# Kernel tuning notes

Hardware: AMD Instinct MI355X
Metric: run time of the kernel (lower is better)

Reference implementation:

```python
import jax, jax.numpy as jnp
import numpy as np

EMBED_DIM = 1024
N_HEADS = 16
HEAD_DIM = EMBED_DIM // N_HEADS
N_CATS = 5
SCALE = float(np.sqrt(HEAD_DIM))


def setup_inputs() -> dict:
    key = jax.random.key(0)
    ks = jax.random.split(key, 16)
    B, S = 2, 2048
    inp = {
        "query": jax.random.normal(ks[0], (B, S, EMBED_DIM), jnp.float32),
        "key_": jax.random.normal(ks[1], (B, S, EMBED_DIM), jnp.float32),
        "value": jax.random.normal(ks[2], (B, S, EMBED_DIM), jnp.float32),
        "responses": jax.random.randint(ks[3], (B, S), 0, N_CATS),
        "mask": jnp.ones((B, S, S), jnp.int32),
        # Linear params (torch convention: y = x @ W.T + b)
        "Wq": jax.random.normal(ks[4], (EMBED_DIM, EMBED_DIM), jnp.float32) * 0.02,
        "bq": jnp.zeros((EMBED_DIM,), jnp.float32),
        "Wk": jax.random.normal(ks[5], (EMBED_DIM, EMBED_DIM), jnp.float32) * 0.02,
        "bk": jnp.zeros((EMBED_DIM,), jnp.float32),
        "Wv": jax.random.normal(ks[6], (EMBED_DIM, EMBED_DIM), jnp.float32) * 0.02,
        "bv": jnp.zeros((EMBED_DIM,), jnp.float32),
        "Wo": jax.random.normal(ks[7], (EMBED_DIM, EMBED_DIM), jnp.float32) * 0.02,
        "bo": jnp.zeros((EMBED_DIM,), jnp.float32),
        # qwk_modulation: Linear(1, n_heads)
        "Wm": jax.random.normal(ks[8], (N_HEADS, 1), jnp.float32) * 0.5,
        "bm": jnp.zeros((N_HEADS,), jnp.float32),
    }
    return inp


def _qwk_matrix():
    i = jnp.arange(N_CATS, dtype=jnp.float32)
    return 1.0 - (i[:, None] - i[None, :]) ** 2 / (N_CATS - 1) ** 2  # [C, C]


def reference(query, key_, value, responses, mask,
              Wq, bq, Wk, bk, Wv, bv, Wo, bo, Wm, bm):
    B, S, E = query.shape
    # projections
    Q = (query @ Wq.T + bq).reshape(B, S, N_HEADS, HEAD_DIM).transpose(0, 2, 1, 3)
    K = (key_ @ Wk.T + bk).reshape(B, S, N_HEADS, HEAD_DIM).transpose(0, 2, 1, 3)
    V = (value @ Wv.T + bv).reshape(B, S, N_HEADS, HEAD_DIM).transpose(0, 2, 1, 3)
    scores = jnp.einsum("bhqd,bhkd->bhqk", Q, K) / SCALE  # [B,H,S,S]
    # QWK ordinal bias: gather pairwise weight, tiny linear 1->H, broadcast-add
    qwk = _qwk_matrix()
    pair = qwk[responses[:, :, None], responses[:, None, :]]  # [B,S,S]
    # Linear(1, n_heads): bias[...,None] @ Wm.T + bm -> [B,S,S,H] -> [B,H,S,S]
    head_bias = pair[:, None, :, :] * Wm[:, 0][None, :, None, None] + bm[None, :, None, None]
    scores = scores + head_bias
    scores = jnp.where(mask[:, None, :, :] == 0, -1e9, scores)
    attn = jax.nn.softmax(scores, axis=-1)
    attended = jnp.einsum("bhqk,bhkd->bhqd", attn, V)
    attended = attended.transpose(0, 2, 1, 3).reshape(B, S, E)
    return attended @ Wo.T + bo
```

## Files before the change

### kernel.cpp

```cpp
#include <hip/hip_runtime.h>
#include <hip/hip_bf16.h>
#include <stdint.h>

#define S_LEN 2048
#define EMB   1024
#define NHEAD 16
#define HDIM  64
#define BATCH 2

typedef __bf16 bf16x8 __attribute__((ext_vector_type(8)));
typedef float  f32x4  __attribute__((ext_vector_type(4)));

__device__ __forceinline__ void gll16(const void* g, void* l) {
  __builtin_amdgcn_global_load_lds(
      (const __attribute__((address_space(1))) void*)g,
      (__attribute__((address_space(3))) void*)l,
      16, 0, 0);
}

__global__ void __launch_bounds__(256) cast_mask_kernel(
    const float* __restrict__ s0, const float* __restrict__ s1, const float* __restrict__ s2,
    const float* __restrict__ s3, const float* __restrict__ s4, const float* __restrict__ s5,
    const float* __restrict__ s6,
    __hip_bfloat16* __restrict__ d0, __hip_bfloat16* __restrict__ d1,
    __hip_bfloat16* __restrict__ d2, __hip_bfloat16* __restrict__ d3,
    __hip_bfloat16* __restrict__ d4, __hip_bfloat16* __restrict__ d5,
    __hip_bfloat16* __restrict__ d6,
    const int* __restrict__ mask, unsigned* __restrict__ flags) {
  const int z = blockIdx.y;
  const int t = threadIdx.x;
  if (z == 7) {
    const int kt = blockIdx.x & 15, qt = (blockIdx.x >> 4) & 31, b = (int)blockIdx.x >> 9;
    const int* base = mask + ((size_t)b * S_LEN + (size_t)qt * 64) * S_LEN + (size_t)kt * 128;
    int ok = 1;
#pragma unroll
    for (int p = 0; p < 8; ++p) {
      int idx = p * 256 + t;
      int row = idx >> 5, c4 = idx & 31;
      const int4 v = *(const int4*)(base + (size_t)row * S_LEN + c4 * 4);
      ok &= (v.x != 0) & (v.y != 0) & (v.z != 0) & (v.w != 0);
    }
    unsigned long long bl = __ballot(ok);
    __shared__ unsigned long long bw[4];
    bw[t >> 6] = bl;
    __syncthreads();
    if (t == 0) {
      unsigned all = ((bw[0] & bw[1] & bw[2] & bw[3]) == ~0ull) ? 1u : 0u;
      flags[((size_t)b * 32 + qt) * 16 + kt] = all;
    }
    return;
  }
  const float* s = (z == 0) ? s0 : (z == 1) ? s1 : (z == 2) ? s2 : (z == 3) ? s3
                 : (z == 4) ? s4 : (z == 5) ? s5 : s6;
  __hip_bfloat16* d = (z == 0) ? d0 : (z == 1) ? d1 : (z == 2) ? d2 : (z == 3) ? d3
                    : (z == 4) ? d4 : (z == 5) ? d5 : d6;
  const int n = (z < 3) ? (BATCH * S_LEN * EMB) : (EMB * EMB);
  const size_t i = ((size_t)blockIdx.x * 256 + t) * 16;
  if (i >= (size_t)n) return;
  __hip_bfloat16 tmp[16];
#pragma unroll
  for (int j = 0; j < 4; ++j) {
    const float4 v = *(const float4*)(s + i + j * 4);
    tmp[j * 4 + 0] = __float2bfloat16(v.x);
    tmp[j * 4 + 1] = __float2bfloat16(v.y);
    tmp[j * 4 + 2] = __float2bfloat16(v.z);
    tmp[j * 4 + 3] = __float2bfloat16(v.w);
  }
  *(bf16x8*)(d + i)     = *(bf16x8*)&tmp[0];
  *(bf16x8*)(d + i + 8) = *(bf16x8*)&tmp[8];
}

__global__ void __launch_bounds__(256, 2)
gemm_kernel(const __hip_bfloat16* __restrict__ A0, const __hip_bfloat16* __restrict__ A1,
            const __hip_bfloat16* __restrict__ A2,
            const __hip_bfloat16* __restrict__ W0, const __hip_bfloat16* __restrict__ W1,
            const __hip_bfloat16* __restrict__ W2,
            const float* __restrict__ b0, const float* __restrict__ b1,
            const float* __restrict__ b2,
            __hip_bfloat16* __restrict__ O0, __hip_bfloat16* __restrict__ O1,
            __hip_bfloat16* __restrict__ O2) {
  __shared__ __align__(16) __hip_bfloat16 As[128 * 32];
  __shared__ __align__(16) __hip_bfloat16 Bs[128 * 32];

  const int z = blockIdx.z;
  const __hip_bfloat16* A  = (z == 0) ? A0 : ((z == 1) ? A1 : A2);
  const __hip_bfloat16* W  = (z == 0) ? W0 : ((z == 1) ? W1 : W2);
  const float* bi          = (z == 0) ? b0 : ((z == 1) ? b1 : b2);
  __hip_bfloat16* O        = (z == 0) ? O0 : ((z == 1) ? O1 : O2);

  const int t = threadIdx.x;
  const int w = t >> 6, lane = t & 63, quad = lane >> 4, l15 = lane & 15;
  const int m0 = blockIdx.y * 128, n0 = blockIdx.x * 128;
  const int wr = w >> 1, wc = w & 1;

  f32x4 acc[4][4];
#pragma unroll
  for (int i = 0; i < 4; ++i)
#pragma unroll
    for (int j = 0; j < 4; ++j) acc[i][j] = (f32x4)0.0f;

  for (int k0 = 0; k0 < EMB; k0 += 32) {
    __syncthreads();
#pragma unroll
    for (int rnd = 0; rnd < 2; ++rnd) {
      int idx = rnd * 256 + t;
      gll16(A + (size_t)(m0 + (idx >> 2)) * EMB + k0 + ((idx & 3) << 3),
            &As[(rnd * 256 + (w << 6)) * 8]);
      gll16(W + (size_t)(n0 + (idx >> 2)) * EMB + k0 + ((idx & 3) << 3),
            &Bs[(rnd * 256 + (w << 6)) * 8]);
    }
    __syncthreads();

    bf16x8 af[4], bfr[4];
#pragma unroll
    for (int i = 0; i < 4; ++i)
      af[i] = *(const bf16x8*)&As[(wr * 64 + i * 16 + l15) * 32 + quad * 8];
#pragma unroll
    for (int j = 0; j < 4; ++j)
      bfr[j] = *(const bf16x8*)&Bs[(wc * 64 + j * 16 + l15) * 32 + quad * 8];
#pragma unroll
    for (int i = 0; i < 4; ++i)
#pragma unroll
      for (int j = 0; j < 4; ++j)
        acc[i][j] = __builtin_amdgcn_mfma_f32_16x16x32_bf16(af[i], bfr[j], acc[i][j], 0, 0, 0);
  }

#pragma unroll
  for (int j = 0; j < 4; ++j) {
    const int ng = n0 + wc * 64 + j * 16 + l15;
    const float bb = bi[ng];
    const int h = ng >> 6, d = ng & 63;
#pragma unroll
    for (int i = 0; i < 4; ++i) {
#pragma unroll
      for (int r = 0; r < 4; ++r) {
        const int mg = m0 + wr * 64 + i * 16 + quad * 4 + r;
        const int b = mg >> 11, s = mg & 2047;
        float v = acc[i][j][r] + bb;
        if (z == 0) {
          O[(((size_t)b * NHEAD + h) * S_LEN + s) * HDIM + d] =
              __float2bfloat16(v * (0.125f * 1.4426950408889634f));
        } else if (z == 1) {
          O[(((size_t)b * NHEAD + h) * S_LEN + s) * HDIM + d] = __float2bfloat16(v);
        } else {
          const size_t idx = (size_t)(b * NHEAD + h) * 131072 + (size_t)(s >> 7) * 8192 +
                             (size_t)((((s >> 5) & 3) * 4 + ((s >> 2) & 3)) * 64 + d) * 8 +
                             ((s >> 4) & 1) * 4 + (s & 3);
          O[idx] = __float2bfloat16(v);
        }
      }
    }
  }
}

__global__ void __launch_bounds__(256, 2)
gemm_o_kernel(const __hip_bfloat16* __restrict__ A, const __hip_bfloat16* __restrict__ W,
              const float* __restrict__ bi, float* __restrict__ O) {
  __shared__ __align__(16) __hip_bfloat16 As[64 * 32];
  __shared__ __align__(16) __hip_bfloat16 Bs[128 * 32];
  const int t = threadIdx.x;
  const int w = t >> 6, lane = t & 63, quad = lane >> 4, l15 = lane & 15;
  const int m0 = blockIdx.y * 64, n0 = blockIdx.x * 128;
  const int wr = w >> 1, wc = w & 1;

  f32x4 acc[2][4];
#pragma unroll
  for (int i = 0; i < 2; ++i)
#pragma unroll
    for (int j = 0; j < 4; ++j) acc[i][j] = (f32x4)0.0f;

  for (int k0 = 0; k0 < EMB; k0 += 32) {
    __syncthreads();
    gll16(A + (size_t)(m0 + (t >> 2)) * EMB + k0 + ((t & 3) << 3), &As[(w << 6) * 8]);
#pragma unroll
    for (int rnd = 0; rnd < 2; ++rnd) {
      int idx = rnd * 256 + t;
      gll16(W + (size_t)(n0 + (idx >> 2)) * EMB + k0 + ((idx & 3) << 3),
            &Bs[(rnd * 256 + (w << 6)) * 8]);
    }
    __syncthreads();

    bf16x8 af[2], bfr[4];
#pragma unroll
    for (int i = 0; i < 2; ++i)
      af[i] = *(const bf16x8*)&As[(wr * 32 + i * 16 + l15) * 32 + quad * 8];
#pragma unroll
    for (int j = 0; j < 4; ++j)
      bfr[j] = *(const bf16x8*)&Bs[(wc * 64 + j * 16 + l15) * 32 + quad * 8];
#pragma unroll
    for (int i = 0; i < 2; ++i)
#pragma unroll
      for (int j = 0; j < 4; ++j)
        acc[i][j] = __builtin_amdgcn_mfma_f32_16x16x32_bf16(af[i], bfr[j], acc[i][j], 0, 0, 0);
  }

#pragma unroll
  for (int j = 0; j < 4; ++j) {
    const int ng = n0 + wc * 64 + j * 16 + l15;
    const float bb = bi[ng];
#pragma unroll
    for (int i = 0; i < 2; ++i) {
#pragma unroll
      for (int r = 0; r < 4; ++r) {
        const int mg = m0 + wr * 32 + i * 16 + quad * 4 + r;
        O[(size_t)mg * EMB + ng] = acc[i][j][r] + bb;
      }
    }
  }
}

__global__ void __launch_bounds__(256, 4)
flash_kernel(const __hip_bfloat16* __restrict__ qws, const __hip_bfloat16* __restrict__ kws,
             const __hip_bfloat16* __restrict__ vpk, const int* __restrict__ responses,
             const int* __restrict__ mask, const float* __restrict__ Wm,
             const unsigned* __restrict__ flags, __hip_bfloat16* __restrict__ att) {
  __shared__ __align__(16) __hip_bfloat16 Ks[128 * 64];
  __shared__ __align__(16) __hip_bfloat16 Vs[8192];
  __shared__ unsigned char rb[S_LEN];

  const int t = threadIdx.x;
  const int w = t >> 6, lane = t & 63, quad = lane >> 4, l15 = lane & 15;
  const int qt = blockIdx.x, h = blockIdx.y, b = blockIdx.z;
  const int bh = b * NHEAD + h;
  const int q0 = qt * 64;

#pragma unroll
  for (int i = 0; i < 8; ++i)
    rb[i * 256 + t] = (unsigned char)responses[b * S_LEN + i * 256 + t];

  const __hip_bfloat16* qbase = qws + ((size_t)bh * S_LEN + q0) * HDIM;
  bf16x8 qf[2];
#pragma unroll
  for (int ks = 0; ks < 2; ++ks)
    qf[ks] = *(const bf16x8*)(qbase + (size_t)(w * 16 + l15) * HDIM + ks * 32 + quad * 8);

  const float c = Wm[h] * (0.0625f * 1.4426950408889634f);
  const float rqf = (float)responses[b * S_LEN + q0 + w * 16 + l15];
  const float A2 = 2.0f * c * rqf;

  const __hip_bfloat16* kptr = kws + ((size_t)bh * S_LEN + (t >> 3)) * HDIM +
                               (((t & 7) ^ ((t >> 3) & 7)) << 3);
  const __hip_bfloat16* vptr = vpk + (size_t)bh * 131072 + (size_t)t * 8;

  float lsum = 0.0f;
  f32x4 acc_o[4];
#pragma unroll
  for (int dt = 0; dt < 4; ++dt) acc_o[dt] = (f32x4)0.0f;

  for (int kt = 0; kt < S_LEN / 128; ++kt) {
    __syncthreads();
#pragma unroll
    for (int p = 0; p < 4; ++p) {
      gll16(kptr + p * 32 * HDIM, &Ks[(p * 256 + (w << 6)) * 8]);
      gll16(vptr + p * 2048,      &Vs[(p * 256 + (w << 6)) * 8]);
    }
    kptr += 128 * HDIM;
    vptr += 8192;
    __syncthreads();

    const unsigned fl = flags[((size_t)b * 32 + qt) * 16 + kt];

    bf16x8 pfr[4];
#pragma unroll
    for (int ct = 0; ct < 8; ++ct) {
      const int rowk = ct * 16 + l15;
      bf16x8 kf0 = *(const bf16x8*)&Ks[rowk * 64 + ((quad ^ (l15 & 7)) << 3)];
      bf16x8 kf1 = *(const bf16x8*)&Ks[rowk * 64 + (((4 + quad) ^ (l15 & 7)) << 3)];
      f32x4 sc = __builtin_amdgcn_mfma_f32_16x16x32_bf16(kf0, qf[0], (f32x4)0.0f, 0, 0, 0);
      sc = __builtin_amdgcn_mfma_f32_16x16x32_bf16(kf1, qf[1], sc, 0, 0, 0);

      const unsigned ru = *(const unsigned*)&rb[kt * 128 + ct * 16 + quad * 4];

      __hip_bfloat16 pb[4];
#pragma unroll
      for (int r = 0; r < 4; ++r) {
        const float rkf = (float)((ru >> (8 * r)) & 255u);
        const float tt = fmaf(-c, rkf, A2);
        const float sb = fmaf(rkf, tt, sc[r]);
        float p = __builtin_amdgcn_exp2f(sb);
        if (!fl) {
          int mq = mask[((size_t)b * S_LEN + q0 + w * 16 + l15) * S_LEN +
                        kt * 128 + ct * 16 + quad * 4 + r];
          p = mq ? p : 0.0f;
        }
        lsum += p;
        pb[r] = __float2bfloat16(p);
      }
      __hip_bfloat16* half = (__hip_bfloat16*)&pfr[ct >> 1] + (ct & 1) * 4;
      half[0] = pb[0]; half[1] = pb[1]; half[2] = pb[2]; half[3] = pb[3];
    }

#pragma unroll
    for (int ct2 = 0; ct2 < 4; ++ct2) {
#pragma unroll
      for (int dt = 0; dt < 4; ++dt) {
        bf16x8 vv = *(const bf16x8*)&Vs[((((ct2 << 2) + quad) << 6) + (dt << 4) + l15) << 3];
        acc_o[dt] = __builtin_amdgcn_mfma_f32_16x16x32_bf16(pfr[ct2], vv, acc_o[dt], 0, 0, 0);
      }
    }
  }

  lsum += __shfl_xor(lsum, 16, 64);
  lsum += __shfl_xor(lsum, 32, 64);
  float inv[4];
#pragma unroll
  for (int r = 0; r < 4; ++r) inv[r] = 1.0f / __shfl(lsum, quad * 4 + r, 64);

#pragma unroll
  for (int dt = 0; dt < 4; ++dt) {
#pragma unroll
    for (int r = 0; r < 4; ++r) {
      float v = acc_o[dt][r] * inv[r];
      att[((size_t)b * S_LEN + q0 + w * 16 + quad * 4 + r) * EMB + h * HDIM + dt * 16 + l15] =
          __float2bfloat16(v);
    }
  }
}

extern "C" void kernel_launch(void* const* d_in, const int* in_sizes, int n_in,
                              void* d_out, int out_size, void* d_ws, size_t ws_size,
                              hipStream_t stream) {
  const float* query = (const float*)d_in[0];
  const float* key_  = (const float*)d_in[1];
  const float* value = (const float*)d_in[2];
  const int* responses = (const int*)d_in[3];
  const int* mask      = (const int*)d_in[4];
  const float* Wq = (const float*)d_in[5];
  const float* bq = (const float*)d_in[6];
  const float* Wk = (const float*)d_in[7];
  const float* bk = (const float*)d_in[8];
  const float* Wv = (const float*)d_in[9];
  const float* bv = (const float*)d_in[10];
  const float* Wo = (const float*)d_in[11];
  const float* bo = (const float*)d_in[12];
  const float* Wm = (const float*)d_in[13];

  __hip_bfloat16* ws = (__hip_bfloat16*)d_ws;
  const size_t NTOK = (size_t)BATCH * S_LEN * EMB;
  const size_t NW   = (size_t)EMB * EMB;
  __hip_bfloat16* qcast = ws;
  __hip_bfloat16* kcast = ws + NTOK;
  __hip_bfloat16* vcast = ws + 2 * NTOK;
  __hip_bfloat16* wqb   = ws + 3 * NTOK;
  __hip_bfloat16* wkb   = wqb + NW;
  __hip_bfloat16* wvb   = wqb + 2 * NW;
  __hip_bfloat16* wob   = wqb + 3 * NW;
  __hip_bfloat16* qws   = wqb + 4 * NW;
  __hip_bfloat16* kws   = qws + NTOK;
  __hip_bfloat16* vpk   = qws + 2 * NTOK;
  __hip_bfloat16* att   = qws + 3 * NTOK;
  unsigned* flags       = (unsigned*)(qws + 4 * NTOK);
  float* out            = (float*)d_out;

  cast_mask_kernel<<<dim3(1024, 8), 256, 0, stream>>>(
      query, key_, value, Wq, Wk, Wv, Wo,
      qcast, kcast, vcast, wqb, wkb, wvb, wob, mask, flags);
  gemm_kernel<<<dim3(8, 32, 3), 256, 0, stream>>>(qcast, kcast, vcast, wqb, wkb, wvb,
                                                  bq, bk, bv, qws, kws, vpk);
  flash_kernel<<<dim3(32, 16, 2), 256, 0, stream>>>(qws, kws, vpk, responses, mask,
                                                    Wm, flags, att);
  gemm_o_kernel<<<dim3(8, 64), 256, 0, stream>>>(att, wob, bo, out);
}
```

Baseline: 262.9 us.

## Widen GEMM K-tile to 64 with swizzled LDS and double flash block size

Both projection GEMMs now stage 64-wide K slices per iteration, with an XOR-swizzled LDS layout so fragment reads avoid bank conflicts, which halves the number of barrier pairs. The flash kernel uses 512-thread blocks covering 128 query rows, so each K/V tile loaded into LDS is shared by twice as many waves. The mask flag for a block is now the AND of the two 64-row flags. The aim is to cut sync and load overhead at the cost of larger LDS use and fewer blocks.

```diff
diff --git a/kernel.cpp b/kernel.cpp
--- a/kernel.cpp
+++ b/kernel.cpp
@@ -79,8 +79,8 @@
             const float* __restrict__ b2,
             __hip_bfloat16* __restrict__ O0, __hip_bfloat16* __restrict__ O1,
             __hip_bfloat16* __restrict__ O2) {
-  __shared__ __align__(16) __hip_bfloat16 As[128 * 32];
-  __shared__ __align__(16) __hip_bfloat16 Bs[128 * 32];
+  __shared__ __align__(16) __hip_bfloat16 As[128 * 64];
+  __shared__ __align__(16) __hip_bfloat16 Bs[128 * 64];
 
   const int z = blockIdx.z;
   const __hip_bfloat16* A  = (z == 0) ? A0 : ((z == 1) ? A1 : A2);
@@ -99,30 +99,43 @@
 #pragma unroll
     for (int j = 0; j < 4; ++j) acc[i][j] = (f32x4)0.0f;
 
-  for (int k0 = 0; k0 < EMB; k0 += 32) {
-    __syncthreads();
-#pragma unroll
-    for (int rnd = 0; rnd < 2; ++rnd) {
-      int idx = rnd * 256 + t;
-      gll16(A + (size_t)(m0 + (idx >> 2)) * EMB + k0 + ((idx & 3) << 3),
-            &As[(rnd * 256 + (w << 6)) * 8]);
-      gll16(W + (size_t)(n0 + (idx >> 2)) * EMB + k0 + ((idx & 3) << 3),
-            &Bs[(rnd * 256 + (w << 6)) * 8]);
-    }
-    __syncthreads();
-
-    bf16x8 af[4], bfr[4];
-#pragma unroll
-    for (int i = 0; i < 4; ++i)
-      af[i] = *(const bf16x8*)&As[(wr * 64 + i * 16 + l15) * 32 + quad * 8];
-#pragma unroll
-    for (int j = 0; j < 4; ++j)
-      bfr[j] = *(const bf16x8*)&Bs[(wc * 64 + j * 16 + l15) * 32 + quad * 8];
-#pragma unroll
-    for (int i = 0; i < 4; ++i)
-#pragma unroll
-      for (int j = 0; j < 4; ++j)
-        acc[i][j] = __builtin_amdgcn_mfma_f32_16x16x32_bf16(af[i], bfr[j], acc[i][j], 0, 0, 0);
+  const int srow = t >> 3;
+  const int scb  = (t & 7) ^ (srow & 7);
+  const __hip_bfloat16* Ap = A + (size_t)(m0 + srow) * EMB + (scb << 3);
+  const __hip_bfloat16* Wp = W + (size_t)(n0 + srow) * EMB + (scb << 3);
+
+  for (int k0 = 0; k0 < EMB; k0 += 64) {
+    __syncthreads();
+#pragma unroll
+    for (int rnd = 0; rnd < 4; ++rnd) {
+      gll16(Ap + (size_t)(rnd * 32) * EMB + k0, &As[(rnd * 256 + (w << 6)) * 8]);
+      gll16(Wp + (size_t)(rnd * 32) * EMB + k0, &Bs[(rnd * 256 + (w << 6)) * 8]);
+    }
+    __syncthreads();
+
+    bf16x8 af[4][2], bfr[4][2];
+#pragma unroll
+    for (int i = 0; i < 4; ++i) {
+      const int ra = wr * 64 + i * 16 + l15;
+#pragma unroll
+      for (int hh = 0; hh < 2; ++hh)
+        af[i][hh] = *(const bf16x8*)&As[ra * 64 + ((((hh << 2) + quad) ^ (l15 & 7)) << 3)];
+    }
+#pragma unroll
+    for (int j = 0; j < 4; ++j) {
+      const int rbw = wc * 64 + j * 16 + l15;
+#pragma unroll
+      for (int hh = 0; hh < 2; ++hh)
+        bfr[j][hh] = *(const bf16x8*)&Bs[rbw * 64 + ((((hh << 2) + quad) ^ (l15 & 7)) << 3)];
+    }
+#pragma unroll
+    for (int hh = 0; hh < 2; ++hh)
+#pragma unroll
+      for (int i = 0; i < 4; ++i)
+#pragma unroll
+        for (int j = 0; j < 4; ++j)
+          acc[i][j] =
+              __builtin_amdgcn_mfma_f32_16x16x32_bf16(af[i][hh], bfr[j][hh], acc[i][j], 0, 0, 0);
   }
 
 #pragma unroll
@@ -156,8 +169,8 @@
 __global__ void __launch_bounds__(256, 2)
 gemm_o_kernel(const __hip_bfloat16* __restrict__ A, const __hip_bfloat16* __restrict__ W,
               const float* __restrict__ bi, float* __restrict__ O) {
-  __shared__ __align__(16) __hip_bfloat16 As[64 * 32];
-  __shared__ __align__(16) __hip_bfloat16 Bs[128 * 32];
+  __shared__ __align__(16) __hip_bfloat16 As[64 * 64];
+  __shared__ __align__(16) __hip_bfloat16 Bs[128 * 64];
   const int t = threadIdx.x;
   const int w = t >> 6, lane = t & 63, quad = lane >> 4, l15 = lane & 15;
   const int m0 = blockIdx.y * 64, n0 = blockIdx.x * 128;
@@ -169,29 +182,44 @@
 #pragma unroll
     for (int j = 0; j < 4; ++j) acc[i][j] = (f32x4)0.0f;
 
-  for (int k0 = 0; k0 < EMB; k0 += 32) {
-    __syncthreads();
-    gll16(A + (size_t)(m0 + (t >> 2)) * EMB + k0 + ((t & 3) << 3), &As[(w << 6) * 8]);
-#pragma unroll
-    for (int rnd = 0; rnd < 2; ++rnd) {
-      int idx = rnd * 256 + t;
-      gll16(W + (size_t)(n0 + (idx >> 2)) * EMB + k0 + ((idx & 3) << 3),
-            &Bs[(rnd * 256 + (w << 6)) * 8]);
-    }
-    __syncthreads();
-
-    bf16x8 af[2], bfr[4];
-#pragma unroll
-    for (int i = 0; i < 2; ++i)
-      af[i] = *(const bf16x8*)&As[(wr * 32 + i * 16 + l15) * 32 + quad * 8];
-#pragma unroll
-    for (int j = 0; j < 4; ++j)
-      bfr[j] = *(const bf16x8*)&Bs[(wc * 64 + j * 16 + l15) * 32 + quad * 8];
-#pragma unroll
-    for (int i = 0; i < 2; ++i)
-#pragma unroll
-      for (int j = 0; j < 4; ++j)
-        acc[i][j] = __builtin_amdgcn_mfma_f32_16x16x32_bf16(af[i], bfr[j], acc[i][j], 0, 0, 0);
+  const int srow = t >> 3;
+  const int scb  = (t & 7) ^ (srow & 7);
+  const __hip_bfloat16* Ap = A + (size_t)(m0 + srow) * EMB + (scb << 3);
+  const __hip_bfloat16* Wp = W + (size_t)(n0 + srow) * EMB + (scb << 3);
+
+  for (int k0 = 0; k0 < EMB; k0 += 64) {
+    __syncthreads();
+#pragma unroll
+    for (int rnd = 0; rnd < 2; ++rnd)
+      gll16(Ap + (size_t)(rnd * 32) * EMB + k0, &As[(rnd * 256 + (w << 6)) * 8]);
+#pragma unroll
+    for (int rnd = 0; rnd < 4; ++rnd)
+      gll16(Wp + (size_t)(rnd * 32) * EMB + k0, &Bs[(rnd * 256 + (w << 6)) * 8]);
+    __syncthreads();
+
+    bf16x8 af[2][2], bfr[4][2];
+#pragma unroll
+    for (int i = 0; i < 2; ++i) {
+      const int ra = wr * 32 + i * 16 + l15;
+#pragma unroll
+      for (int hh = 0; hh < 2; ++hh)
+        af[i][hh] = *(const bf16x8*)&As[ra * 64 + ((((hh << 2) + quad) ^ (l15 & 7)) << 3)];
+    }
+#pragma unroll
+    for (int j = 0; j < 4; ++j) {
+      const int rbw = wc * 64 + j * 16 + l15;
+#pragma unroll
+      for (int hh = 0; hh < 2; ++hh)
+        bfr[j][hh] = *(const bf16x8*)&Bs[rbw * 64 + ((((hh << 2) + quad) ^ (l15 & 7)) << 3)];
+    }
+#pragma unroll
+    for (int hh = 0; hh < 2; ++hh)
+#pragma unroll
+      for (int i = 0; i < 2; ++i)
+#pragma unroll
+        for (int j = 0; j < 4; ++j)
+          acc[i][j] =
+              __builtin_amdgcn_mfma_f32_16x16x32_bf16(af[i][hh], bfr[j][hh], acc[i][j], 0, 0, 0);
   }
 
 #pragma unroll
@@ -209,7 +237,7 @@
   }
 }
 
-__global__ void __launch_bounds__(256, 4)
+__global__ void __launch_bounds__(512, 4)
 flash_kernel(const __hip_bfloat16* __restrict__ qws, const __hip_bfloat16* __restrict__ kws,
              const __hip_bfloat16* __restrict__ vpk, const int* __restrict__ responses,
              const int* __restrict__ mask, const float* __restrict__ Wm,
@@ -222,11 +250,11 @@
   const int w = t >> 6, lane = t & 63, quad = lane >> 4, l15 = lane & 15;
   const int qt = blockIdx.x, h = blockIdx.y, b = blockIdx.z;
   const int bh = b * NHEAD + h;
-  const int q0 = qt * 64;
-
-#pragma unroll
-  for (int i = 0; i < 8; ++i)
-    rb[i * 256 + t] = (unsigned char)responses[b * S_LEN + i * 256 + t];
+  const int q0 = qt * 128;
+
+#pragma unroll
+  for (int i = 0; i < 4; ++i)
+    rb[i * 512 + t] = (unsigned char)responses[b * S_LEN + i * 512 + t];
 
   const __hip_bfloat16* qbase = qws + ((size_t)bh * S_LEN + q0) * HDIM;
   bf16x8 qf[2];
@@ -250,15 +278,16 @@
   for (int kt = 0; kt < S_LEN / 128; ++kt) {
     __syncthreads();
 #pragma unroll
-    for (int p = 0; p < 4; ++p) {
-      gll16(kptr + p * 32 * HDIM, &Ks[(p * 256 + (w << 6)) * 8]);
-      gll16(vptr + p * 2048,      &Vs[(p * 256 + (w << 6)) * 8]);
+    for (int p = 0; p < 2; ++p) {
+      gll16(kptr + p * 64 * HDIM, &Ks[(p * 512 + (w << 6)) * 8]);
+      gll16(vptr + p * 4096,      &Vs[(p * 512 + (w << 6)) * 8]);
     }
     kptr += 128 * HDIM;
     vptr += 8192;
     __syncthreads();
 
-    const unsigned fl = flags[((size_t)b * 32 + qt) * 16 + kt];
+    const unsigned fl = flags[((size_t)b * 32 + 2 * qt) * 16 + kt] &
+                        flags[((size_t)b * 32 + 2 * qt + 1) * 16 + kt];
 
     bf16x8 pfr[4];
 #pragma unroll
@@ -357,7 +386,7 @@
       qcast, kcast, vcast, wqb, wkb, wvb, wob, mask, flags);
   gemm_kernel<<<dim3(8, 32, 3), 256, 0, stream>>>(qcast, kcast, vcast, wqb, wkb, wvb,
                                                   bq, bk, bv, qws, kws, vpk);
-  flash_kernel<<<dim3(32, 16, 2), 256, 0, stream>>>(qws, kws, vpk, responses, mask,
+  flash_kernel<<<dim3(16, 16, 2), 512, 0, stream>>>(qws, kws, vpk, responses, mask,
                                                     Wm, flags, att);
   gemm_o_kernel<<<dim3(8, 64), 256, 0, stream>>>(att, wob, bo, out);
 }
```

After: 254.8 us. -3.1%, faster.
